# Kernel optimization log

Hardware: AMD Instinct MI355X
Metric: run time of the kernel (lower is better)

Reference implementation:

```python
import jax, jax.numpy as jnp
import numpy as np

E, V, F_, B = 8192, 2048, 2048, 8
H, DEC, EDGE, META = 128, 128, 2, 4
MEMH, MEMAGG, AGGH = 256, 128, 128
IN_DIM = DEC + EDGE + META  # 134


def _incidence(idx, n):
    # dense (n, E) 0/1 incidence matrix, as used by torch.mm in the original
    return jnp.zeros((n, idx.shape[0]), jnp.float32).at[idx, jnp.arange(idx.shape[0])].set(1.0)


def setup_inputs() -> dict:
    key = jax.random.key(0)
    ks = jax.random.split(key, 32)
    var_idx = jax.random.randint(ks[0], (E,), 0, V)          # variable of each edge
    fun_idx = jax.random.randint(ks[1], (E,), 0, F_)         # clause of each edge
    batch_of_var = jax.random.randint(ks[2], (V,), 0, B)     # problem id of each variable
    variable_mask = _incidence(var_idx, V)                   # (V, E)
    function_mask = _incidence(fun_idx, F_)                  # (F, E)
    b_variable_mask = jnp.zeros((V, B), jnp.float32).at[jnp.arange(V), batch_of_var].set(1.0)

    def lin(k, i, o):
        kw, kb = jax.random.split(k)
        return (jax.random.normal(kw, (i, o), jnp.float32) * 0.05,
                jax.random.normal(kb, (o,), jnp.float32) * 0.05)

    p = {}
    for pre, k0 in (("v", 10), ("f", 20)):
        p[pre + "M1w"], p[pre + "M1b"] = lin(ks[k0], IN_DIM, MEMH)
        p[pre + "M2w"], p[pre + "M2b"] = lin(ks[k0 + 1], MEMH, MEMAGG)
        p[pre + "A1w"], p[pre + "A1b"] = lin(ks[k0 + 2], MEMAGG + EDGE, AGGH)
        p[pre + "A2w"], p[pre + "A2b"] = lin(ks[k0 + 3], AGGH, H)

    return dict(
        variable_state=jax.random.normal(ks[3], (E, H), jnp.float32),
        function_state=jax.random.normal(ks[4], (E, H), jnp.float32),
        decimator_variable_state=jax.random.normal(ks[5], (E, DEC), jnp.float32),
        decimator_function_state=jax.random.normal(ks[6], (E, DEC), jnp.float32),
        edge_feature=jax.random.normal(ks[7], (E, EDGE), jnp.float32),
        meta_data=jax.random.normal(ks[8], (B, META), jnp.float32),
        active_mask=jax.random.randint(ks[9], (B, 1), 0, 2),
        variable_mask=variable_mask, variable_mask_t=variable_mask.T,
        function_mask=function_mask, function_mask_t=function_mask.T,
        b_variable_mask=b_variable_mask,
        **p,
    )


def _aggregate(state, feature, mask, mask_t, W1, b1, W2, b2, A1, c1, A2, c2):
    # MessageAggregator (include_self_message=False, edge_mask=None)
    h = jax.nn.relu(state @ W1 + b1)       # (E, MEMH)  pre-aggregation transform
    h = h @ W2 + b2                        # (E, MEMAGG)
    agg = mask_t @ (mask @ h) - h          # node-sum broadcast back to edges, minus self message
    a = jax.nn.relu(jnp.concatenate([agg, feature], 1) @ A1 + c1)  # post-agg transform
    return a @ A2 + c2                     # (E, H)


def reference(variable_state, function_state, decimator_variable_state,
              decimator_function_state, edge_feature, meta_data, active_mask,
              variable_mask, variable_mask_t, function_mask, function_mask_t,
              b_variable_mask,
              vM1w, vM1b, vM2w, vM2b, vA1w, vA1b, vA2w, vA2b,
              fM1w, fM1b, fM2w, fM2b, fA1w, fA1b, fA2w, fA2b):
    # active mask broadcast: batch -> variables -> edges (dense mm chain as in torch)
    mask = variable_mask_t @ (b_variable_mask @ active_mask.astype(jnp.float32))  # (E, 1)
    # meta-data broadcast: batch -> variables -> edges
    graph_feat = variable_mask_t @ (b_variable_mask @ meta_data)                  # (E, META)

    dvs = jnp.concatenate([decimator_variable_state, edge_feature, graph_feat], 1)
    agg_v = _aggregate(dvs, edge_feature, variable_mask, variable_mask_t,
                       vM1w, vM1b, vM2w, vM2b, vA1w, vA1b, vA2w, vA2b)
    function_state = mask * agg_v + (1.0 - mask) * function_state  # dropout: identity (eval)

    dfs = jnp.concatenate([decimator_function_state, edge_feature, graph_feat], 1)
    agg_f = _aggregate(dfs, edge_feature, function_mask, function_mask_t,
                       fM1w, fM1b, fM2w, fM2b, fA1w, fA1b, fA2w, fA2b)
    variable_state = mask * agg_f + (1.0 - mask) * variable_state

    return (variable_state, function_state)
```

## Files before the change

kernel.cpp:

```cpp
#include <hip/hip_runtime.h>

#define E_N 8192
#define V_N 2048
#define F_N 2048
#define B_N 8
#define H_N 128
#define DEC_N 128
#define EDGE_N 2
#define META_N 4
#define IN_DIM 134
#define MEMH 256
#define MEMAGG 128
#define AGGH 128

typedef __attribute__((ext_vector_type(8))) short short8;
typedef __attribute__((ext_vector_type(4))) float f32x4;

__device__ inline unsigned short f2bf(float x) {
    unsigned u = __float_as_uint(x);
    unsigned r = (u + 0x7FFFu + ((u >> 16) & 1u)) >> 16;
    return (unsigned short)r;
}

__device__ inline short8 pack8(float4 u0, float4 u1) {
    short8 s;
    s[0] = (short)f2bf(u0.x); s[1] = (short)f2bf(u0.y);
    s[2] = (short)f2bf(u0.z); s[3] = (short)f2bf(u0.w);
    s[4] = (short)f2bf(u1.x); s[5] = (short)f2bf(u1.y);
    s[6] = (short)f2bf(u1.z); s[7] = (short)f2bf(u1.w);
    return s;
}

__global__ void k_bov(const float* __restrict__ bvm, int* __restrict__ bov) {
    int v = blockIdx.x * blockDim.x + threadIdx.x;
    if (v < V_N) {
        float s = 0.f;
#pragma unroll
        for (int b = 0; b < B_N; ++b) s += bvm[v * B_N + b] * (float)b;
        bov[v] = (int)(s + 0.5f);
    }
}

__global__ __launch_bounds__(256) void k_idx(const float* __restrict__ vmt,
                                             const float* __restrict__ fmt,
                                             int* __restrict__ vidx,
                                             int* __restrict__ fidx,
                                             const int* __restrict__ bov,
                                             const int* __restrict__ active,
                                             const float* __restrict__ meta,
                                             float* __restrict__ emask,
                                             float* __restrict__ gfeat) {
    int wave = (int)((blockIdx.x * blockDim.x + threadIdx.x) >> 6);
    int lane = threadIdx.x & 63;
    const float* m;
    int* out;
    int e;
    bool isVar = wave < E_N;
    if (isVar) { m = vmt; out = vidx; e = wave; }
    else       { m = fmt; out = fidx; e = wave - E_N; }
    const float4* row = (const float4*)(m + (size_t)e * V_N);
    for (int base = 0; base < V_N / 4; base += 64) {
        float4 v = row[base + lane];
        int hit = -1;
        int c = (base + lane) * 4;
        if      (v.x != 0.f) hit = c;
        else if (v.y != 0.f) hit = c + 1;
        else if (v.z != 0.f) hit = c + 2;
        else if (v.w != 0.f) hit = c + 3;
        unsigned long long bm = __ballot(hit >= 0);
        if (bm) {
            int src = __ffsll((long long)bm) - 1;
            int val = __shfl(hit, src);
            if (lane == 0) {
                out[e] = val;
                if (isVar) {
                    int b = bov[val];
                    emask[e] = (float)active[b];
                    ((float4*)gfeat)[e] = ((const float4*)meta)[b];
                }
            }
            break;
        }
    }
}

struct RDesc { const float* src; unsigned short* dst; int K; int N; int Kp; };
struct RPack { RDesc d[8]; float* nszero; };

__global__ __launch_bounds__(256) void k_repack(RPack p) {
    int gid = (int)((blockIdx.y * gridDim.x + blockIdx.x) * 256 + threadIdx.x);
    const int NZ4 = (V_N + F_N) * MEMAGG / 4;
    if (gid < NZ4) ((float4*)p.nszero)[gid] = (float4){0.f, 0.f, 0.f, 0.f};

    RDesc d = p.d[blockIdx.y];
    int i = blockIdx.x * 256 + threadIdx.x;
    int total = d.Kp * d.N;
    if (i >= total) return;
    int elem = i & 7;
    int lane = (i >> 3) & 63;
    int f    = i >> 9;
    int c16n = d.N >> 4;
    int c16 = f % c16n, kc = f / c16n;
    int k = kc * 32 + (lane >> 4) * 8 + elem;
    int c = c16 * 16 + (lane & 15);
    float v = (k < d.K) ? d.src[(size_t)k * d.N + c] : 0.f;
    d.dst[i] = f2bf(v);
}

struct F1Args {
    const float* dec[2];
    const float* ef;
    const float* gfeat;
    const unsigned short* wpack[2];
    const float* b1[2];
    const float* b2[2];
    const int* idx[2];
    float* h2[2];
    float* ns[2];
};

__global__ __launch_bounds__(256) void k_fused1(F1Args A) {
    int br = blockIdx.y;
    const float* dec = A.dec[br];
    const unsigned short* W1f = A.wpack[br];
    const unsigned short* W2f = A.wpack[br] + 160 * 256;
    const float* b1 = A.b1[br];
    const float* b2 = A.b2[br];
    const int* idx = A.idx[br];
    float* h2o = A.h2[br];
    float* ns  = A.ns[br];

    int tid = threadIdx.x;
    int wave = tid >> 6, lane = tid & 63;
    int lrow = lane & 15, lgrp = lane >> 4;
    int e0 = blockIdx.x * 32;

    __shared__ unsigned short h1s[32 * 256];

    int n0 = wave * 64;
    f32x4 acc1[2][4];
#pragma unroll
    for (int nt = 0; nt < 4; ++nt) {
        float bv = b1[n0 + nt * 16 + lrow];
#pragma unroll
        for (int mt = 0; mt < 2; ++mt) acc1[mt][nt] = (f32x4){bv, bv, bv, bv};
    }
    const float4* dec4 = (const float4*)dec;
#pragma unroll
    for (int kc = 0; kc < 5; ++kc) {
        short8 a[2];
#pragma unroll
        for (int mt = 0; mt < 2; ++mt) {
            int r = e0 + mt * 16 + lrow;
            if (kc < 4) {
                float4 u0 = dec4[(size_t)r * 32 + kc * 8 + lgrp * 2];
                float4 u1 = dec4[(size_t)r * 32 + kc * 8 + lgrp * 2 + 1];
                a[mt] = pack8(u0, u1);
            } else {
                short8 z = (short8)0;
                if (lgrp == 0) {
                    z[0] = (short)f2bf(A.ef[r * 2]);
                    z[1] = (short)f2bf(A.ef[r * 2 + 1]);
                    z[2] = (short)f2bf(A.gfeat[r * 4]);
                    z[3] = (short)f2bf(A.gfeat[r * 4 + 1]);
                    z[4] = (short)f2bf(A.gfeat[r * 4 + 2]);
                    z[5] = (short)f2bf(A.gfeat[r * 4 + 3]);
                }
                a[mt] = z;
            }
        }
#pragma unroll
        for (int nt = 0; nt < 4; ++nt) {
            short8 b = *(const short8*)(W1f + ((size_t)(kc * 16 + (n0 >> 4) + nt) * 64 + lane) * 8);
#pragma unroll
            for (int mt = 0; mt < 2; ++mt)
                acc1[mt][nt] = __builtin_amdgcn_mfma_f32_16x16x32_bf16(a[mt], b, acc1[mt][nt], 0, 0, 0);
        }
    }
#pragma unroll
    for (int mt = 0; mt < 2; ++mt)
#pragma unroll
        for (int nt = 0; nt < 4; ++nt)
#pragma unroll
            for (int j = 0; j < 4; ++j) {
                int row = mt * 16 + lgrp * 4 + j;
                int col = n0 + nt * 16 + lrow;
                h1s[row * 256 + (col ^ ((row & 7) << 3))] = f2bf(fmaxf(acc1[mt][nt][j], 0.f));
            }
    __syncthreads();

    int c0 = wave * 32;
    f32x4 acc2[2][2];
#pragma unroll
    for (int nt = 0; nt < 2; ++nt) {
        float bv = b2[c0 + nt * 16 + lrow];
#pragma unroll
        for (int mt = 0; mt < 2; ++mt) acc2[mt][nt] = (f32x4){bv, bv, bv, bv};
    }
#pragma unroll
    for (int kc = 0; kc < 8; ++kc) {
        short8 a2[2];
#pragma unroll
        for (int mt = 0; mt < 2; ++mt) {
            int r = mt * 16 + lrow;
            int kb = kc * 32 + lgrp * 8;
            a2[mt] = *(const short8*)(h1s + r * 256 + (kb ^ ((r & 7) << 3)));
        }
#pragma unroll
        for (int nt = 0; nt < 2; ++nt) {
            short8 b = *(const short8*)(W2f + ((size_t)(kc * 8 + (c0 >> 4) + nt) * 64 + lane) * 8);
#pragma unroll
            for (int mt = 0; mt < 2; ++mt)
                acc2[mt][nt] = __builtin_amdgcn_mfma_f32_16x16x32_bf16(a2[mt], b, acc2[mt][nt], 0, 0, 0);
        }
    }
#pragma unroll
    for (int mt = 0; mt < 2; ++mt)
#pragma unroll
        for (int nt = 0; nt < 2; ++nt) {
            int col = c0 + nt * 16 + lrow;
#pragma unroll
            for (int j = 0; j < 4; ++j) {
                int row = e0 + mt * 16 + lgrp * 4 + j;
                float v = acc2[mt][nt][j];
                h2o[(size_t)row * 128 + col] = v;
                atomicAdd(ns + (size_t)idx[row] * 128 + col, v);
            }
        }
}

struct F2Args {
    const unsigned short* wpack[2];
    const float* c1[2];
    const float* c2[2];
    const float* h2[2];
    const float* ns[2];
    const int* idx[2];
    const float* ef;
    const float* emask;
    const float* oldst[2];
    float* outst[2];
};

__global__ __launch_bounds__(256) void k_fused2(F2Args A) {
    int br = blockIdx.y;
    const unsigned short* A1f = A.wpack[br] + 160 * 256 + 256 * 128;
    const unsigned short* A2f = A1f + 160 * 128;
    const float* c1 = A.c1[br];
    const float* c2 = A.c2[br];
    const float* h2 = A.h2[br];
    const float* ns = A.ns[br];
    const int* idx = A.idx[br];
    const float* oldst = A.oldst[br];
    float* outst = A.outst[br];

    int tid = threadIdx.x;
    int wave = tid >> 6, lane = tid & 63;
    int lrow = lane & 15, lgrp = lane >> 4;
    int e0 = blockIdx.x * 32;

    __shared__ unsigned short as_[32 * 128];

    int n0 = wave * 32;
    f32x4 accp[2][2];
#pragma unroll
    for (int nt = 0; nt < 2; ++nt) {
        float bv = c1[n0 + nt * 16 + lrow];
#pragma unroll
        for (int mt = 0; mt < 2; ++mt) accp[mt][nt] = (f32x4){bv, bv, bv, bv};
    }
    const float4* ns4 = (const float4*)ns;
    const float4* h24 = (const float4*)h2;
#pragma unroll
    for (int kc = 0; kc < 5; ++kc) {
        short8 a[2];
#pragma unroll
        for (int mt = 0; mt < 2; ++mt) {
            int r = e0 + mt * 16 + lrow;
            if (kc < 4) {
                int node = idx[r];
                float4 u0 = ns4[(size_t)node * 32 + kc * 8 + lgrp * 2];
                float4 u1 = ns4[(size_t)node * 32 + kc * 8 + lgrp * 2 + 1];
                float4 v0 = h24[(size_t)r * 32 + kc * 8 + lgrp * 2];
                float4 v1 = h24[(size_t)r * 32 + kc * 8 + lgrp * 2 + 1];
                float4 d0 = {u0.x - v0.x, u0.y - v0.y, u0.z - v0.z, u0.w - v0.w};
                float4 d1 = {u1.x - v1.x, u1.y - v1.y, u1.z - v1.z, u1.w - v1.w};
                a[mt] = pack8(d0, d1);
            } else {
                short8 z = (short8)0;
                if (lgrp == 0) {
                    z[0] = (short)f2bf(A.ef[r * 2]);
                    z[1] = (short)f2bf(A.ef[r * 2 + 1]);
                }
                a[mt] = z;
            }
        }
#pragma unroll
        for (int nt = 0; nt < 2; ++nt) {
            short8 b = *(const short8*)(A1f + ((size_t)(kc * 8 + (n0 >> 4) + nt) * 64 + lane) * 8);
#pragma unroll
            for (int mt = 0; mt < 2; ++mt)
                accp[mt][nt] = __builtin_amdgcn_mfma_f32_16x16x32_bf16(a[mt], b, accp[mt][nt], 0, 0, 0);
        }
    }
#pragma unroll
    for (int mt = 0; mt < 2; ++mt)
#pragma unroll
        for (int nt = 0; nt < 2; ++nt)
#pragma unroll
            for (int j = 0; j < 4; ++j) {
                int row = mt * 16 + lgrp * 4 + j;
                int col = n0 + nt * 16 + lrow;
                as_[row * 128 + (col ^ ((row & 7) << 3))] = f2bf(fmaxf(accp[mt][nt][j], 0.f));
            }
    __syncthreads();

    f32x4 acco[2][2];
#pragma unroll
    for (int nt = 0; nt < 2; ++nt) {
        float bv = c2[n0 + nt * 16 + lrow];
#pragma unroll
        for (int mt = 0; mt < 2; ++mt) acco[mt][nt] = (f32x4){bv, bv, bv, bv};
    }
#pragma unroll
    for (int kc = 0; kc < 4; ++kc) {
        short8 a2[2];
#pragma unroll
        for (int mt = 0; mt < 2; ++mt) {
            int r = mt * 16 + lrow;
            int kb = kc * 32 + lgrp * 8;
            a2[mt] = *(const short8*)(as_ + r * 128 + (kb ^ ((r & 7) << 3)));
        }
#pragma unroll
        for (int nt = 0; nt < 2; ++nt) {
            short8 b = *(const short8*)(A2f + ((size_t)(kc * 8 + (n0 >> 4) + nt) * 64 + lane) * 8);
#pragma unroll
            for (int mt = 0; mt < 2; ++mt)
                acco[mt][nt] = __builtin_amdgcn_mfma_f32_16x16x32_bf16(a2[mt], b, acco[mt][nt], 0, 0, 0);
        }
    }
#pragma unroll
    for (int mt = 0; mt < 2; ++mt)
#pragma unroll
        for (int nt = 0; nt < 2; ++nt) {
            int col = n0 + nt * 16 + lrow;
#pragma unroll
            for (int j = 0; j < 4; ++j) {
                int row = e0 + mt * 16 + lgrp * 4 + j;
                float m = A.emask[row];
                float old = oldst[(size_t)row * 128 + col];
                outst[(size_t)row * 128 + col] = m * acco[mt][nt][j] + (1.f - m) * old;
            }
        }
}

extern "C" void kernel_launch(void* const* d_in, const int* in_sizes, int n_in,
                              void* d_out, int out_size, void* d_ws, size_t ws_size,
                              hipStream_t stream) {
    const float* variable_state = (const float*)d_in[0];
    const float* function_state = (const float*)d_in[1];
    const float* dec_v          = (const float*)d_in[2];
    const float* dec_f          = (const float*)d_in[3];
    const float* ef             = (const float*)d_in[4];
    const float* meta           = (const float*)d_in[5];
    const int*   active         = (const int*)d_in[6];
    const float* vmask_t        = (const float*)d_in[8];
    const float* fmask_t        = (const float*)d_in[10];
    const float* bvm            = (const float*)d_in[11];
    const float* vM1w = (const float*)d_in[12]; const float* vM1b = (const float*)d_in[13];
    const float* vM2w = (const float*)d_in[14]; const float* vM2b = (const float*)d_in[15];
    const float* vA1w = (const float*)d_in[16]; const float* vA1b = (const float*)d_in[17];
    const float* vA2w = (const float*)d_in[18]; const float* vA2b = (const float*)d_in[19];
    const float* fM1w = (const float*)d_in[20]; const float* fM1b = (const float*)d_in[21];
    const float* fM2w = (const float*)d_in[22]; const float* fM2b = (const float*)d_in[23];
    const float* fA1w = (const float*)d_in[24]; const float* fA1b = (const float*)d_in[25];
    const float* fA2w = (const float*)d_in[26]; const float* fA2b = (const float*)d_in[27];

    float* out_vs = (float*)d_out;
    float* out_fs = (float*)d_out + (size_t)E_N * H_N;

    int*   var_idx = (int*)d_ws;
    int*   fun_idx = var_idx + E_N;
    int*   bov     = fun_idx + E_N;
    float* emask   = (float*)(bov + V_N);
    float* gfeat   = emask + E_N;
    float* hv2     = gfeat + (size_t)E_N * 4;
    float* hf2     = hv2 + (size_t)E_N * MEMAGG;
    float* nsv     = hf2 + (size_t)E_N * MEMAGG;
    float* nsf     = nsv + (size_t)V_N * MEMAGG;
    unsigned short* wpack = (unsigned short*)(nsf + (size_t)F_N * MEMAGG);
    const int PBR = 160 * 256 + 256 * 128 + 160 * 128 + 128 * 128;
    unsigned short* wpv = wpack;
    unsigned short* wpf = wpack + PBR;

    RPack rp;
    rp.d[0] = {vM1w, wpv,                          IN_DIM, MEMH,   160};
    rp.d[1] = {vM2w, wpv + 160 * 256,              MEMH,   MEMAGG, 256};
    rp.d[2] = {vA1w, wpv + 160 * 256 + 256 * 128,  130,    AGGH,   160};
    rp.d[3] = {vA2w, wpv + 160 * 256 + 256 * 128 + 160 * 128, 128, H_N, 128};
    rp.d[4] = {fM1w, wpf,                          IN_DIM, MEMH,   160};
    rp.d[5] = {fM2w, wpf + 160 * 256,              MEMH,   MEMAGG, 256};
    rp.d[6] = {fA1w, wpf + 160 * 256 + 256 * 128,  130,    AGGH,   160};
    rp.d[7] = {fA2w, wpf + 160 * 256 + 256 * 128 + 160 * 128, 128, H_N, 128};
    rp.nszero = nsv;
    k_repack<<<dim3(160, 8), 256, 0, stream>>>(rp);

    k_bov<<<(V_N + 255) / 256, 256, 0, stream>>>(bvm, bov);
    k_idx<<<(2 * E_N) / 4, 256, 0, stream>>>(vmask_t, fmask_t, var_idx, fun_idx,
                                             bov, active, meta, emask, gfeat);

    F1Args f1;
    f1.dec[0] = dec_v;  f1.dec[1] = dec_f;
    f1.ef = ef;         f1.gfeat = gfeat;
    f1.wpack[0] = wpv;  f1.wpack[1] = wpf;
    f1.b1[0] = vM1b;    f1.b1[1] = fM1b;
    f1.b2[0] = vM2b;    f1.b2[1] = fM2b;
    f1.idx[0] = var_idx; f1.idx[1] = fun_idx;
    f1.h2[0] = hv2;     f1.h2[1] = hf2;
    f1.ns[0] = nsv;     f1.ns[1] = nsf;
    k_fused1<<<dim3(E_N / 32, 2), 256, 0, stream>>>(f1);

    F2Args f2;
    f2.wpack[0] = wpv;  f2.wpack[1] = wpf;
    f2.c1[0] = vA1b;    f2.c1[1] = fA1b;
    f2.c2[0] = vA2b;    f2.c2[1] = fA2b;
    f2.h2[0] = hv2;     f2.h2[1] = hf2;
    f2.ns[0] = nsv;     f2.ns[1] = nsf;
    f2.idx[0] = var_idx; f2.idx[1] = fun_idx;
    f2.ef = ef;         f2.emask = emask;
    f2.oldst[0] = function_state;  f2.oldst[1] = variable_state;
    f2.outst[0] = out_fs;          f2.outst[1] = out_vs;
    k_fused2<<<dim3(E_N / 32, 2), 256, 0, stream>>>(f2);
}
```

Measured before the change: 64.41 us.

## Merge setup kernels, batch index-search loads, halve MLP row tiles

```diff
diff --git a/kernel.cpp b/kernel.cpp
--- a/kernel.cpp
+++ b/kernel.cpp
@@ -31,64 +31,21 @@
     return s;
 }
 
-__global__ void k_bov(const float* __restrict__ bvm, int* __restrict__ bov) {
-    int v = blockIdx.x * blockDim.x + threadIdx.x;
-    if (v < V_N) {
-        float s = 0.f;
-#pragma unroll
-        for (int b = 0; b < B_N; ++b) s += bvm[v * B_N + b] * (float)b;
-        bov[v] = (int)(s + 0.5f);
-    }
-}
-
-__global__ __launch_bounds__(256) void k_idx(const float* __restrict__ vmt,
-                                             const float* __restrict__ fmt,
-                                             int* __restrict__ vidx,
-                                             int* __restrict__ fidx,
-                                             const int* __restrict__ bov,
-                                             const int* __restrict__ active,
-                                             const float* __restrict__ meta,
-                                             float* __restrict__ emask,
-                                             float* __restrict__ gfeat) {
-    int wave = (int)((blockIdx.x * blockDim.x + threadIdx.x) >> 6);
-    int lane = threadIdx.x & 63;
-    const float* m;
-    int* out;
-    int e;
-    bool isVar = wave < E_N;
-    if (isVar) { m = vmt; out = vidx; e = wave; }
-    else       { m = fmt; out = fidx; e = wave - E_N; }
-    const float4* row = (const float4*)(m + (size_t)e * V_N);
-    for (int base = 0; base < V_N / 4; base += 64) {
-        float4 v = row[base + lane];
-        int hit = -1;
-        int c = (base + lane) * 4;
-        if      (v.x != 0.f) hit = c;
-        else if (v.y != 0.f) hit = c + 1;
-        else if (v.z != 0.f) hit = c + 2;
-        else if (v.w != 0.f) hit = c + 3;
-        unsigned long long bm = __ballot(hit >= 0);
-        if (bm) {
-            int src = __ffsll((long long)bm) - 1;
-            int val = __shfl(hit, src);
-            if (lane == 0) {
-                out[e] = val;
-                if (isVar) {
-                    int b = bov[val];
-                    emask[e] = (float)active[b];
-                    ((float4*)gfeat)[e] = ((const float4*)meta)[b];
-                }
-            }
-            break;
-        }
-    }
-}
-
 struct RDesc { const float* src; unsigned short* dst; int K; int N; int Kp; };
-struct RPack { RDesc d[8]; float* nszero; };
-
-__global__ __launch_bounds__(256) void k_repack(RPack p) {
-    int gid = (int)((blockIdx.y * gridDim.x + blockIdx.x) * 256 + threadIdx.x);
+struct SetupArgs { RDesc d[8]; float* nszero; const float* bvm; int* bov; };
+
+__global__ __launch_bounds__(256) void k_setup(SetupArgs p) {
+    if (blockIdx.y == 8) {
+        if (blockIdx.x < 8) {
+            int v = blockIdx.x * 256 + threadIdx.x;
+            float s = 0.f;
+#pragma unroll
+            for (int b = 0; b < B_N; ++b) s += p.bvm[v * B_N + b] * (float)b;
+            p.bov[v] = (int)(s + 0.5f);
+        }
+        return;
+    }
+    int gid = (int)((blockIdx.y * 160 + blockIdx.x) * 256 + threadIdx.x);
     const int NZ4 = (V_N + F_N) * MEMAGG / 4;
     if (gid < NZ4) ((float4*)p.nszero)[gid] = (float4){0.f, 0.f, 0.f, 0.f};
 
@@ -107,6 +64,58 @@
     d.dst[i] = f2bf(v);
 }
 
+__global__ __launch_bounds__(256) void k_idx(const float* __restrict__ vmt,
+                                             const float* __restrict__ fmt,
+                                             int* __restrict__ vidx,
+                                             int* __restrict__ fidx,
+                                             const int* __restrict__ bov,
+                                             const int* __restrict__ active,
+                                             const float* __restrict__ meta,
+                                             float* __restrict__ emask,
+                                             float* __restrict__ gfeat) {
+    int wave = (int)((blockIdx.x * blockDim.x + threadIdx.x) >> 6);
+    int lane = threadIdx.x & 63;
+    bool isVar = wave < E_N;
+    const float* m = isVar ? vmt : fmt;
+    int* out = isVar ? vidx : fidx;
+    int e = isVar ? wave : wave - E_N;
+    const float4* row = (const float4*)(m + (size_t)e * V_N);
+
+    int pos = -1;
+#pragma unroll
+    for (int half = 0; half < 2; ++half) {
+        if (pos < 0) {
+            float4 v0 = row[half * 256 + lane];
+            float4 v1 = row[half * 256 + 64 + lane];
+            float4 v2 = row[half * 256 + 128 + lane];
+            float4 v3 = row[half * 256 + 192 + lane];
+            int hit = -1;
+            float4 vv[4] = {v0, v1, v2, v3};
+#pragma unroll
+            for (int j = 0; j < 4; ++j) {
+                float4 v = vv[j];
+                int c = (half * 256 + j * 64 + lane) * 4;
+                if (hit < 0) {
+                    if      (v.x != 0.f) hit = c;
+                    else if (v.y != 0.f) hit = c + 1;
+                    else if (v.z != 0.f) hit = c + 2;
+                    else if (v.w != 0.f) hit = c + 3;
+                }
+            }
+            unsigned long long bm = __ballot(hit >= 0);
+            if (bm) pos = __shfl(hit, __ffsll((long long)bm) - 1);
+        }
+    }
+    if (lane == 0) {
+        out[e] = pos;
+        if (isVar) {
+            int b = bov[pos];
+            emask[e] = (float)active[b];
+            ((float4*)gfeat)[e] = ((const float4*)meta)[b];
+        }
+    }
+}
+
 struct F1Args {
     const float* dec[2];
     const float* ef;
@@ -133,100 +142,83 @@
     int tid = threadIdx.x;
     int wave = tid >> 6, lane = tid & 63;
     int lrow = lane & 15, lgrp = lane >> 4;
-    int e0 = blockIdx.x * 32;
-
-    __shared__ unsigned short h1s[32 * 256];
+    int e0 = blockIdx.x * 16;
+
+    __shared__ unsigned short h1s[16 * 256];
 
     int n0 = wave * 64;
-    f32x4 acc1[2][4];
+    f32x4 acc1[4];
 #pragma unroll
     for (int nt = 0; nt < 4; ++nt) {
         float bv = b1[n0 + nt * 16 + lrow];
-#pragma unroll
-        for (int mt = 0; mt < 2; ++mt) acc1[mt][nt] = (f32x4){bv, bv, bv, bv};
+        acc1[nt] = (f32x4){bv, bv, bv, bv};
     }
     const float4* dec4 = (const float4*)dec;
+    int r = e0 + lrow;
 #pragma unroll
     for (int kc = 0; kc < 5; ++kc) {
-        short8 a[2];
-#pragma unroll
-        for (int mt = 0; mt < 2; ++mt) {
-            int r = e0 + mt * 16 + lrow;
-            if (kc < 4) {
-                float4 u0 = dec4[(size_t)r * 32 + kc * 8 + lgrp * 2];
-                float4 u1 = dec4[(size_t)r * 32 + kc * 8 + lgrp * 2 + 1];
-                a[mt] = pack8(u0, u1);
-            } else {
-                short8 z = (short8)0;
-                if (lgrp == 0) {
-                    z[0] = (short)f2bf(A.ef[r * 2]);
-                    z[1] = (short)f2bf(A.ef[r * 2 + 1]);
-                    z[2] = (short)f2bf(A.gfeat[r * 4]);
-                    z[3] = (short)f2bf(A.gfeat[r * 4 + 1]);
-                    z[4] = (short)f2bf(A.gfeat[r * 4 + 2]);
-                    z[5] = (short)f2bf(A.gfeat[r * 4 + 3]);
-                }
-                a[mt] = z;
+        short8 a;
+        if (kc < 4) {
+            float4 u0 = dec4[(size_t)r * 32 + kc * 8 + lgrp * 2];
+            float4 u1 = dec4[(size_t)r * 32 + kc * 8 + lgrp * 2 + 1];
+            a = pack8(u0, u1);
+        } else {
+            short8 z = (short8)0;
+            if (lgrp == 0) {
+                z[0] = (short)f2bf(A.ef[r * 2]);
+                z[1] = (short)f2bf(A.ef[r * 2 + 1]);
+                z[2] = (short)f2bf(A.gfeat[r * 4]);
+                z[3] = (short)f2bf(A.gfeat[r * 4 + 1]);
+                z[4] = (short)f2bf(A.gfeat[r * 4 + 2]);
+                z[5] = (short)f2bf(A.gfeat[r * 4 + 3]);
             }
+            a = z;
         }
 #pragma unroll
         for (int nt = 0; nt < 4; ++nt) {
             short8 b = *(const short8*)(W1f + ((size_t)(kc * 16 + (n0 >> 4) + nt) * 64 + lane) * 8);
-#pragma unroll
-            for (int mt = 0; mt < 2; ++mt)
-                acc1[mt][nt] = __builtin_amdgcn_mfma_f32_16x16x32_bf16(a[mt], b, acc1[mt][nt], 0, 0, 0);
-        }
-    }
-#pragma unroll
-    for (int mt = 0; mt < 2; ++mt)
-#pragma unroll
-        for (int nt = 0; nt < 4; ++nt)
-#pragma unroll
-            for (int j = 0; j < 4; ++j) {
-                int row = mt * 16 + lgrp * 4 + j;
-                int col = n0 + nt * 16 + lrow;
-                h1s[row * 256 + (col ^ ((row & 7) << 3))] = f2bf(fmaxf(acc1[mt][nt][j], 0.f));
-            }
+            acc1[nt] = __builtin_amdgcn_mfma_f32_16x16x32_bf16(a, b, acc1[nt], 0, 0, 0);
+        }
+    }
+#pragma unroll
+    for (int nt = 0; nt < 4; ++nt)
+#pragma unroll
+        for (int j = 0; j < 4; ++j) {
+            int row = lgrp * 4 + j;
+            int col = n0 + nt * 16 + lrow;
+            h1s[row * 256 + (col ^ ((row & 7) << 3))] = f2bf(fmaxf(acc1[nt][j], 0.f));
+        }
     __syncthreads();
 
     int c0 = wave * 32;
-    f32x4 acc2[2][2];
+    f32x4 acc2[2];
 #pragma unroll
     for (int nt = 0; nt < 2; ++nt) {
         float bv = b2[c0 + nt * 16 + lrow];
-#pragma unroll
-        for (int mt = 0; mt < 2; ++mt) acc2[mt][nt] = (f32x4){bv, bv, bv, bv};
+        acc2[nt] = (f32x4){bv, bv, bv, bv};
     }
 #pragma unroll
     for (int kc = 0; kc < 8; ++kc) {
-        short8 a2[2];
-#pragma unroll
-        for (int mt = 0; mt < 2; ++mt) {
-            int r = mt * 16 + lrow;
-            int kb = kc * 32 + lgrp * 8;
-            a2[mt] = *(const short8*)(h1s + r * 256 + (kb ^ ((r & 7) << 3)));
-        }
+        int kb = kc * 32 + lgrp * 8;
+        short8 a2 = *(const short8*)(h1s + lrow * 256 + (kb ^ ((lrow & 7) << 3)));
 #pragma unroll
         for (int nt = 0; nt < 2; ++nt) {
             short8 b = *(const short8*)(W2f + ((size_t)(kc * 8 + (c0 >> 4) + nt) * 64 + lane) * 8);
-#pragma unroll
-            for (int mt = 0; mt < 2; ++mt)
-                acc2[mt][nt] = __builtin_amdgcn_mfma_f32_16x16x32_bf16(a2[mt], b, acc2[mt][nt], 0, 0, 0);
-        }
-    }
-#pragma unroll
-    for (int mt = 0; mt < 2; ++mt)
+            acc2[nt] = __builtin_amdgcn_mfma_f32_16x16x32_bf16(a2, b, acc2[nt], 0, 0, 0);
+        }
+    }
+#pragma unroll
+    for (int j = 0; j < 4; ++j) {
+        int row = e0 + lgrp * 4 + j;
+        int node = idx[row];
 #pragma unroll
         for (int nt = 0; nt < 2; ++nt) {
             int col = c0 + nt * 16 + lrow;
-#pragma unroll
-            for (int j = 0; j < 4; ++j) {
-                int row = e0 + mt * 16 + lgrp * 4 + j;
-                float v = acc2[mt][nt][j];
-                h2o[(size_t)row * 128 + col] = v;
-                atomicAdd(ns + (size_t)idx[row] * 128 + col, v);
-            }
-        }
+            float v = acc2[nt][j];
+            h2o[(size_t)row * 128 + col] = v;
+            atomicAdd(ns + (size_t)node * 128 + col, v);
+        }
+    }
 }
 
 struct F2Args {
@@ -257,101 +249,83 @@
     int tid = threadIdx.x;
     int wave = tid >> 6, lane = tid & 63;
     int lrow = lane & 15, lgrp = lane >> 4;
-    int e0 = blockIdx.x * 32;
-
-    __shared__ unsigned short as_[32 * 128];
+    int e0 = blockIdx.x * 16;
+
+    __shared__ unsigned short as_[16 * 128];
 
     int n0 = wave * 32;
-    f32x4 accp[2][2];
+    f32x4 accp[2];
 #pragma unroll
     for (int nt = 0; nt < 2; ++nt) {
         float bv = c1[n0 + nt * 16 + lrow];
-#pragma unroll
-        for (int mt = 0; mt < 2; ++mt) accp[mt][nt] = (f32x4){bv, bv, bv, bv};
+        accp[nt] = (f32x4){bv, bv, bv, bv};
     }
     const float4* ns4 = (const float4*)ns;
     const float4* h24 = (const float4*)h2;
+    int r = e0 + lrow;
+    int node = idx[r];
 #pragma unroll
     for (int kc = 0; kc < 5; ++kc) {
-        short8 a[2];
-#pragma unroll
-        for (int mt = 0; mt < 2; ++mt) {
-            int r = e0 + mt * 16 + lrow;
-            if (kc < 4) {
-                int node = idx[r];
-                float4 u0 = ns4[(size_t)node * 32 + kc * 8 + lgrp * 2];
-                float4 u1 = ns4[(size_t)node * 32 + kc * 8 + lgrp * 2 + 1];
-                float4 v0 = h24[(size_t)r * 32 + kc * 8 + lgrp * 2];
-                float4 v1 = h24[(size_t)r * 32 + kc * 8 + lgrp * 2 + 1];
-                float4 d0 = {u0.x - v0.x, u0.y - v0.y, u0.z - v0.z, u0.w - v0.w};
-                float4 d1 = {u1.x - v1.x, u1.y - v1.y, u1.z - v1.z, u1.w - v1.w};
-                a[mt] = pack8(d0, d1);
-            } else {
-                short8 z = (short8)0;
-                if (lgrp == 0) {
-                    z[0] = (short)f2bf(A.ef[r * 2]);
-                    z[1] = (short)f2bf(A.ef[r * 2 + 1]);
-                }
-                a[mt] = z;
+        short8 a;
+        if (kc < 4) {
+            float4 u0 = ns4[(size_t)node * 32 + kc * 8 + lgrp * 2];
+            float4 u1 = ns4[(size_t)node * 32 + kc * 8 + lgrp * 2 + 1];
+            float4 v0 = h24[(size_t)r * 32 + kc * 8 + lgrp * 2];
+            float4 v1 = h24[(size_t)r * 32 + kc * 8 + lgrp * 2 + 1];
+            float4 d0 = {u0.x - v0.x, u0.y - v0.y, u0.z - v0.z, u0.w - v0.w};
+            float4 d1 = {u1.x - v1.x, u1.y - v1.y, u1.z - v1.z, u1.w - v1.w};
+            a = pack8(d0, d1);
+        } else {
+            short8 z = (short8)0;
+            if (lgrp == 0) {
+                z[0] = (short)f2bf(A.ef[r * 2]);
+                z[1] = (short)f2bf(A.ef[r * 2 + 1]);
             }
+            a = z;
         }
 #pragma unroll
         for (int nt = 0; nt < 2; ++nt) {
             short8 b = *(const short8*)(A1f + ((size_t)(kc * 8 + (n0 >> 4) + nt) * 64 + lane) * 8);
-#pragma unroll
-            for (int mt = 0; mt < 2; ++mt)
-                accp[mt][nt] = __builtin_amdgcn_mfma_f32_16x16x32_bf16(a[mt], b, accp[mt][nt], 0, 0, 0);
-        }
-    }
-#pragma unroll
-    for (int mt = 0; mt < 2; ++mt)
-#pragma unroll
-        for (int nt = 0; nt < 2; ++nt)
-#pragma unroll
-            for (int j = 0; j < 4; ++j) {
-                int row = mt * 16 + lgrp * 4 + j;
-                int col = n0 + nt * 16 + lrow;
-                as_[row * 128 + (col ^ ((row & 7) << 3))] = f2bf(fmaxf(accp[mt][nt][j], 0.f));
-            }
+            accp[nt] = __builtin_amdgcn_mfma_f32_16x16x32_bf16(a, b, accp[nt], 0, 0, 0);
+        }
+    }
+#pragma unroll
+    for (int nt = 0; nt < 2; ++nt)
+#pragma unroll
+        for (int j = 0; j < 4; ++j) {
+            int row = lgrp * 4 + j;
+            int col = n0 + nt * 16 + lrow;
+            as_[row * 128 + (col ^ ((row & 7) << 3))] = f2bf(fmaxf(accp[nt][j], 0.f));
+        }
     __syncthreads();
 
-    f32x4 acco[2][2];
+    f32x4 acco[2];
 #pragma unroll
     for (int nt = 0; nt < 2; ++nt) {
         float bv = c2[n0 + nt * 16 + lrow];
-#pragma unroll
-        for (int mt = 0; mt < 2; ++mt) acco[mt][nt] = (f32x4){bv, bv, bv, bv};
+        acco[nt] = (f32x4){bv, bv, bv, bv};
     }
 #pragma unroll
     for (int kc = 0; kc < 4; ++kc) {
-        short8 a2[2];
-#pragma unroll
-        for (int mt = 0; mt < 2; ++mt) {
-            int r = mt * 16 + lrow;
-            int kb = kc * 32 + lgrp * 8;
-            a2[mt] = *(const short8*)(as_ + r * 128 + (kb ^ ((r & 7) << 3)));
-        }
+        int kb = kc * 32 + lgrp * 8;
+        short8 a2 = *(const short8*)(as_ + lrow * 128 + (kb ^ ((lrow & 7) << 3)));
 #pragma unroll
         for (int nt = 0; nt < 2; ++nt) {
             short8 b = *(const short8*)(A2f + ((size_t)(kc * 8 + (n0 >> 4) + nt) * 64 + lane) * 8);
-#pragma unroll
-            for (int mt = 0; mt < 2; ++mt)
-                acco[mt][nt] = __builtin_amdgcn_mfma_f32_16x16x32_bf16(a2[mt], b, acco[mt][nt], 0, 0, 0);
-        }
-    }
-#pragma unroll
-    for (int mt = 0; mt < 2; ++mt)
+            acco[nt] = __builtin_amdgcn_mfma_f32_16x16x32_bf16(a2, b, acco[nt], 0, 0, 0);
+        }
+    }
+#pragma unroll
+    for (int j = 0; j < 4; ++j) {
+        int row = e0 + lgrp * 4 + j;
+        float m = A.emask[row];
 #pragma unroll
         for (int nt = 0; nt < 2; ++nt) {
             int col = n0 + nt * 16 + lrow;
-#pragma unroll
-            for (int j = 0; j < 4; ++j) {
-                int row = e0 + mt * 16 + lgrp * 4 + j;
-                float m = A.emask[row];
-                float old = oldst[(size_t)row * 128 + col];
-                outst[(size_t)row * 128 + col] = m * acco[mt][nt][j] + (1.f - m) * old;
-            }
-        }
+            float old = oldst[(size_t)row * 128 + col];
+            outst[(size_t)row * 128 + col] = m * acco[nt][j] + (1.f - m) * old;
+        }
+    }
 }
 
 extern "C" void kernel_launch(void* const* d_in, const int* in_sizes, int n_in,
@@ -393,19 +367,20 @@
     unsigned short* wpv = wpack;
     unsigned short* wpf = wpack + PBR;
 
-    RPack rp;
-    rp.d[0] = {vM1w, wpv,                          IN_DIM, MEMH,   160};
-    rp.d[1] = {vM2w, wpv + 160 * 256,              MEMH,   MEMAGG, 256};
-    rp.d[2] = {vA1w, wpv + 160 * 256 + 256 * 128,  130,    AGGH,   160};
-    rp.d[3] = {vA2w, wpv + 160 * 256 + 256 * 128 + 160 * 128, 128, H_N, 128};
-    rp.d[4] = {fM1w, wpf,                          IN_DIM, MEMH,   160};
-    rp.d[5] = {fM2w, wpf + 160 * 256,              MEMH,   MEMAGG, 256};
-    rp.d[6] = {fA1w, wpf + 160 * 256 + 256 * 128,  130,    AGGH,   160};
-    rp.d[7] = {fA2w, wpf + 160 * 256 + 256 * 128 + 160 * 128, 128, H_N, 128};
-    rp.nszero = nsv;
-    k_repack<<<dim3(160, 8), 256, 0, stream>>>(rp);
-
-    k_bov<<<(V_N + 255) / 256, 256, 0, stream>>>(bvm, bov);
+    SetupArgs sp;
+    sp.d[0] = {vM1w, wpv,                          IN_DIM, MEMH,   160};
+    sp.d[1] = {vM2w, wpv + 160 * 256,              MEMH,   MEMAGG, 256};
+    sp.d[2] = {vA1w, wpv + 160 * 256 + 256 * 128,  130,    AGGH,   160};
+    sp.d[3] = {vA2w, wpv + 160 * 256 + 256 * 128 + 160 * 128, 128, H_N, 128};
+    sp.d[4] = {fM1w, wpf,                          IN_DIM, MEMH,   160};
+    sp.d[5] = {fM2w, wpf + 160 * 256,              MEMH,   MEMAGG, 256};
+    sp.d[6] = {fA1w, wpf + 160 * 256 + 256 * 128,  130,    AGGH,   160};
+    sp.d[7] = {fA2w, wpf + 160 * 256 + 256 * 128 + 160 * 128, 128, H_N, 128};
+    sp.nszero = nsv;
+    sp.bvm = bvm;
+    sp.bov = bov;
+    k_setup<<<dim3(160, 9), 256, 0, stream>>>(sp);
+
     k_idx<<<(2 * E_N) / 4, 256, 0, stream>>>(vmask_t, fmask_t, var_idx, fun_idx,
                                              bov, active, meta, emask, gfeat);
 
@@ -418,7 +393,7 @@
     f1.idx[0] = var_idx; f1.idx[1] = fun_idx;
     f1.h2[0] = hv2;     f1.h2[1] = hf2;
     f1.ns[0] = nsv;     f1.ns[1] = nsf;
-    k_fused1<<<dim3(E_N / 32, 2), 256, 0, stream>>>(f1);
+    k_fused1<<<dim3(E_N / 16, 2), 256, 0, stream>>>(f1);
 
     F2Args f2;
     f2.wpack[0] = wpv;  f2.wpack[1] = wpf;
@@ -430,5 +405,5 @@
     f2.ef = ef;         f2.emask = emask;
     f2.oldst[0] = function_state;  f2.oldst[1] = variable_state;
     f2.outst[0] = out_fs;          f2.outst[1] = out_vs;
-    k_fused2<<<dim3(E_N / 32, 2), 256, 0, stream>>>(f2);
-}
+    k_fused2<<<dim3(E_N / 16, 2), 256, 0, stream>>>(f2);
+}
```

Result: faster. 58.37 us (-9.4%).
